# Performance work log

Hardware: AMD Instinct MI355X
Metric: run time of the kernel (lower is better)

Reference implementation:

```python
import jax, jax.numpy as jnp
import numpy as np

B, S, E, H, K, V = 128, 1024, 512, 512, 2, 32000


def setup_inputs() -> dict:
    key = jax.random.key(0)
    k0, k1, k2, k3, k4, k5 = jax.random.split(key, 6)
    scale = 1.0 / np.sqrt(H)  # torch LSTMCell init range
    inp = jax.random.randint(k0, (B, S), 0, V, dtype=jnp.int32)
    input_embed = jax.random.normal(k1, (B, S, E), dtype=jnp.float32)
    # one LSTMCell parameter set per expert cell, stacked on leading K axis
    W_ih = jax.random.uniform(k2, (K, 4 * H, E), jnp.float32, -scale, scale)
    W_hh = jax.random.uniform(k3, (K, 4 * H, H), jnp.float32, -scale, scale)
    b_ih = jax.random.uniform(k4, (K, 4 * H), jnp.float32, -scale, scale)
    b_hh = jax.random.uniform(k5, (K, 4 * H), jnp.float32, -scale, scale)
    return {"input": inp, "input_embed": input_embed,
            "W_ih": W_ih, "W_hh": W_hh, "b_ih": b_ih, "b_hh": b_hh}


def reference(input, input_embed, W_ih, W_hh, b_ih, b_hh):
    # assignments: vocab id -> cell id via modulo (covers the whole vocab)
    num_cells = W_ih.shape[0]
    batch, seq_len, _ = input_embed.shape
    hidden_size = W_hh.shape[-1]
    cell_map = (input % num_cells).astype(jnp.int32)  # [B, S]
    bias = (b_ih + b_hh)[:, None, :]                   # [K, 1, 4H]
    bidx = jnp.arange(batch)

    xs = (jnp.swapaxes(input_embed, 0, 1),  # [S, B, E]
          jnp.swapaxes(cell_map, 0, 1))     # [S, B]

    def step(carry, x):
        h, c = carry
        x_t, k_t = x
        # compute gates for every cell, then pick the routed one per token
        gates = (jnp.einsum('be,kge->kbg', x_t, W_ih)
                 + jnp.einsum('bh,kgh->kbg', h, W_hh)
                 + bias)                      # [K, B, 4H]
        g = gates[k_t, bidx]                  # [B, 4H] routed selection
        i, f, gg, o = jnp.split(g, 4, axis=-1)
        c_new = jax.nn.sigmoid(f) * c + jax.nn.sigmoid(i) * jnp.tanh(gg)
        h_new = jax.nn.sigmoid(o) * jnp.tanh(c_new)
        return (h_new, c_new), h_new

    h0 = jnp.zeros((batch, hidden_size), jnp.float32)
    c0 = jnp.zeros((batch, hidden_size), jnp.float32)
    (h_last, c_last), outs = jax.lax.scan(step, (h0, c0), xs)
    combined_outputs = jnp.swapaxes(outs, 0, 1)  # [B, S, H]
    return combined_outputs, (h_last, c_last)
```

## Files before the change

### kernel.cpp

```cpp
#include <hip/hip_runtime.h>
#include <hip/hip_bf16.h>

typedef __bf16 bf16x8 __attribute__((ext_vector_type(8)));
typedef float f32x4 __attribute__((ext_vector_type(4)));
typedef unsigned long long u64;

#define B_ 128
#define S_ 1024
#define E_ 512
#define H_ 512
#define TOK 32
#define KROWS 64
#define WSTRIDE 1032
#define GSTR 65
#define NGRP 4
#define WPG 64
#define FSTR 16
#define SMEM_BYTES (KROWS * WSTRIDE * 2 + 64 * 4 + TOK * GSTR * 4)

__device__ __forceinline__ float sigf(float x) { return 1.0f / (1.0f + __expf(-x)); }

__device__ __forceinline__ bf16x8 cvt8(float4 a, float4 b) {
    bf16x8 r;
    r[0] = (__bf16)a.x; r[1] = (__bf16)a.y; r[2] = (__bf16)a.z; r[3] = (__bf16)a.w;
    r[4] = (__bf16)b.x; r[5] = (__bf16)b.y; r[6] = (__bf16)b.z; r[7] = (__bf16)b.w;
    return r;
}

union bfpack { u64 q[2]; bf16x8 v; };
union bfbits { __hip_bfloat16 b; unsigned short s; };

__global__ void init_ws_kernel(unsigned int* bar) {
    for (int i = threadIdx.x; i < NGRP * WPG * FSTR; i += 256) bar[i] = 0u;
}

__global__ void __launch_bounds__(512, 2)
lstm_kernel(const int* __restrict__ inp, const float* __restrict__ embed,
            const float* __restrict__ Wih, const float* __restrict__ Whh,
            const float* __restrict__ bih, const float* __restrict__ bhh,
            float* __restrict__ out, unsigned int* __restrict__ bar,
            __hip_bfloat16* __restrict__ hbuf)
{
    extern __shared__ char smem[];
    __hip_bfloat16* wbuf = (__hip_bfloat16*)smem;
    float* bias_l = (float*)(smem + KROWS * WSTRIDE * 2);
    float* gbuf   = bias_l + 64;

    const int tid = threadIdx.x;
    const int bid = blockIdx.x;
    const int grp = bid & 3;
    const int r   = bid >> 2;
    const int j0  = r * 8;

    for (int it = tid; it < KROWS * 256; it += 512) {
        int n = it >> 8;
        int q = it & 255;
        int cell = n >> 5, rem = n & 31, gate = rem >> 3, jj = rem & 7;
        size_t grow = (size_t)(cell * 2048 + gate * 512 + j0 + jj);
        float4 v;
        int dstoff;
        if (q < 128) { v = ((const float4*)(Wih + grow * E_))[q];       dstoff = q * 4; }
        else         { v = ((const float4*)(Whh + grow * H_))[q - 128]; dstoff = 512 + (q - 128) * 4; }
        __hip_bfloat16* dst = wbuf + n * WSTRIDE + dstoff;
        dst[0] = __float2bfloat16(v.x); dst[1] = __float2bfloat16(v.y);
        dst[2] = __float2bfloat16(v.z); dst[3] = __float2bfloat16(v.w);
    }
    if (tid < 64) {
        int n = tid, cell = n >> 5, rem = n & 31, gate = rem >> 3, jj = rem & 7;
        size_t off = (size_t)cell * 2048 + gate * 512 + j0 + jj;
        bias_l[tid] = bih[off] + bhh[off];
    }
    __syncthreads();

    const int lane = tid & 63, wid = tid >> 6;
    const int lm = lane & 15, quad = lane >> 4;
    const int mtile = wid & 1, rho = wid >> 1;
    const int tokA = grp * TOK + mtile * 16 + lm;
    const float* xbase = embed + (size_t)tokA * S_ * E_ + quad * 8;
    const __hip_bfloat16* wx = wbuf + (rho * 16 + lm) * WSTRIDE + quad * 8;
    const __hip_bfloat16* wh = wx + 512;
    const float bv = bias_l[rho * 16 + lm];
    const __hip_bfloat16* hbA = hbuf + (size_t)tokA * H_ + quad * 8;

    const int b_loc = (tid >> 3) & 31, jj = tid & 7;
    const int b_glob = grp * TOK + b_loc;
    const int* inpp = inp + (size_t)b_glob * S_;
    float* outp = out + (size_t)b_glob * S_ * H_ + j0 + jj;
    __hip_bfloat16* hwp = hbuf + (size_t)b_glob * H_ + j0 + jj;
    float creg = 0.0f, hlast = 0.0f;

    volatile unsigned int* myflag = bar + (grp * WPG + r) * FSTR;
    volatile const unsigned int* pollp = bar + (grp * WPG + lane) * FSTR;

    f32x4 acc_next;
    {
        f32x4 ax = {bv, bv, bv, bv};
        const float* xp = xbase;
#pragma unroll
        for (int ks = 0; ks < 16; ++ks) {
            float4 f0 = *(const float4*)(xp + ks * 32);
            float4 f1 = *(const float4*)(xp + ks * 32 + 4);
            bf16x8 a = cvt8(f0, f1);
            bf16x8 b = *(const bf16x8*)(wx + ks * 32);
            ax = __builtin_amdgcn_mfma_f32_16x16x32_bf16(a, b, ax, 0, 0, 0);
        }
        acc_next = ax;
    }
    int cell_next = inpp[0];

    for (int t = 0; t < S_; ++t) {
        f32x4 acc = acc_next;
        const int cell_cur = cell_next;

        if (t > 0) {
            const volatile u64* hp = (const volatile u64*)(hbA + (size_t)(t & 1) * B_ * H_);
#pragma unroll
            for (int ks = 0; ks < 16; ++ks) {
                bfpack u;
                u.q[0] = hp[ks * 8];
                u.q[1] = hp[ks * 8 + 1];
                bf16x8 b = *(const bf16x8*)(wh + ks * 32);
                acc = __builtin_amdgcn_mfma_f32_16x16x32_bf16(u.v, b, acc, 0, 0, 0);
            }
        }

        {
            float* gp = gbuf + (mtile * 16 + quad * 4) * GSTR + rho * 16 + lm;
            gp[0] = acc[0]; gp[GSTR] = acc[1]; gp[2 * GSTR] = acc[2]; gp[3 * GSTR] = acc[3];
        }
        __syncthreads();

        if (tid < 256) {
            int cell = cell_cur & 1;
            const float* gb = gbuf + b_loc * GSTR + cell * 32 + jj;
            float iv = gb[0], fv = gb[8], gv = gb[16], ov = gb[24];
            creg  = sigf(fv) * creg + sigf(iv) * tanhf(gv);
            hlast = sigf(ov) * tanhf(creg);
            bfbits cv; cv.b = __float2bfloat16(hlast);
            *(volatile unsigned short*)(hwp + (size_t)((t + 1) & 1) * B_ * H_) = cv.s;
        }

        __syncthreads();
        if (tid == 0) *myflag = (unsigned int)(t + 1);

        if (tid < 256) outp[(size_t)t * H_] = hlast;
        {
            int tn = (t + 1 < S_) ? (t + 1) : (S_ - 1);
            cell_next = inpp[tn];
        }
        {
            f32x4 ax = {bv, bv, bv, bv};
            if (t + 1 < S_) {
                const float* xp = xbase + (size_t)(t + 1) * E_;
#pragma unroll
                for (int ks = 0; ks < 16; ++ks) {
                    float4 f0 = *(const float4*)(xp + ks * 32);
                    float4 f1 = *(const float4*)(xp + ks * 32 + 4);
                    bf16x8 a = cvt8(f0, f1);
                    bf16x8 b = *(const bf16x8*)(wx + ks * 32);
                    ax = __builtin_amdgcn_mfma_f32_16x16x32_bf16(a, b, ax, 0, 0, 0);
                }
            }
            acc_next = ax;
        }

        if (wid == 0) {
            const unsigned int tgt = (unsigned int)(t + 1);
            unsigned int guard = 0;
            while (!__all((int)(*pollp >= tgt))) {
                __builtin_amdgcn_s_sleep(4);
                if (++guard > 0x02000000u) break;
            }
        }
        __syncthreads();
    }

    if (tid < 256) {
        size_t base = (size_t)B_ * S_ * H_;
        out[base + (size_t)b_glob * H_ + j0 + jj] = hlast;
        out[base + (size_t)B_ * H_ + (size_t)b_glob * H_ + j0 + jj] = creg;
    }
}

extern "C" void kernel_launch(void* const* d_in, const int* in_sizes, int n_in,
                              void* d_out, int out_size, void* d_ws, size_t ws_size,
                              hipStream_t stream) {
    const int* inp     = (const int*)d_in[0];
    const float* embed = (const float*)d_in[1];
    const float* Wih   = (const float*)d_in[2];
    const float* Whh   = (const float*)d_in[3];
    const float* bih   = (const float*)d_in[4];
    const float* bhh   = (const float*)d_in[5];
    float* out         = (float*)d_out;

    unsigned int* bar    = (unsigned int*)d_ws;
    __hip_bfloat16* hbuf = (__hip_bfloat16*)((char*)d_ws + 16384);

    static_assert(SMEM_BYTES <= 160 * 1024, "LDS overflow");
    hipFuncSetAttribute((const void*)lstm_kernel,
                        hipFuncAttributeMaxDynamicSharedMemorySize, SMEM_BYTES);

    hipLaunchKernelGGL(init_ws_kernel, dim3(1), dim3(256), 0, stream, bar);
    hipLaunchKernelGGL(lstm_kernel, dim3(256), dim3(512), SMEM_BYTES, stream,
                       inp, embed, Wih, Whh, bih, bhh, out, bar, hbuf);
}
```

Baseline: 16.77 ms.

## Split hidden columns across 512 workgroups and use hierarchical per-group barrier

Halves the hidden-unit slice per workgroup (4 columns instead of 8), launching 512 workgroups of 256 threads so the grid covers more CUs with smaller LDS weight tiles. The grid-wide step barrier becomes two-level: one leader block per batch group polls all 128 peer flags and then publishes a single group flag that the other blocks poll, with a shorter sleep. This is meant to spread the recurrent matmul and gate work across more compute and to cut polling traffic. In exchange there are more blocks to synchronise and an extra hop of latency through the leader on every timestep.

After: 17.56 ms. 4.7% more time.

```diff
diff --git a/kernel.cpp b/kernel.cpp
--- a/kernel.cpp
+++ b/kernel.cpp
@@ -10,13 +10,14 @@
 #define E_ 512
 #define H_ 512
 #define TOK 32
-#define KROWS 64
+#define KROWS 32
+#define JW 4
 #define WSTRIDE 1032
-#define GSTR 65
+#define GSTR 33
 #define NGRP 4
-#define WPG 64
+#define WPG 128
 #define FSTR 16
-#define SMEM_BYTES (KROWS * WSTRIDE * 2 + 64 * 4 + TOK * GSTR * 4)
+#define SMEM_BYTES (KROWS * WSTRIDE * 2 + KROWS * 4 + TOK * GSTR * 4)
 
 __device__ __forceinline__ float sigf(float x) { return 1.0f / (1.0f + __expf(-x)); }
 
@@ -31,10 +32,10 @@
 union bfbits { __hip_bfloat16 b; unsigned short s; };
 
 __global__ void init_ws_kernel(unsigned int* bar) {
-    for (int i = threadIdx.x; i < NGRP * WPG * FSTR; i += 256) bar[i] = 0u;
-}
-
-__global__ void __launch_bounds__(512, 2)
+    for (int i = threadIdx.x; i < (NGRP * WPG + NGRP) * FSTR; i += 256) bar[i] = 0u;
+}
+
+__global__ void __launch_bounds__(256, 2)
 lstm_kernel(const int* __restrict__ inp, const float* __restrict__ embed,
             const float* __restrict__ Wih, const float* __restrict__ Whh,
             const float* __restrict__ bih, const float* __restrict__ bhh,
@@ -44,19 +45,19 @@
     extern __shared__ char smem[];
     __hip_bfloat16* wbuf = (__hip_bfloat16*)smem;
     float* bias_l = (float*)(smem + KROWS * WSTRIDE * 2);
-    float* gbuf   = bias_l + 64;
+    float* gbuf   = bias_l + KROWS;
 
     const int tid = threadIdx.x;
     const int bid = blockIdx.x;
-    const int grp = bid & 3;
-    const int r   = bid >> 2;
-    const int j0  = r * 8;
-
-    for (int it = tid; it < KROWS * 256; it += 512) {
+    const int grp = (bid + (bid >> 8)) & 3;
+    const int r   = ((bid >> 8) << 6) + ((bid & 255) >> 2);
+    const int j0  = r * JW;
+
+    for (int it = tid; it < KROWS * 256; it += 256) {
         int n = it >> 8;
         int q = it & 255;
-        int cell = n >> 5, rem = n & 31, gate = rem >> 3, jj = rem & 7;
-        size_t grow = (size_t)(cell * 2048 + gate * 512 + j0 + jj);
+        int cell = n >> 4, gate = (n >> 2) & 3, jjj = n & 3;
+        size_t grow = (size_t)(cell * 2048 + gate * 512 + j0 + jjj);
         float4 v;
         int dstoff;
         if (q < 128) { v = ((const float4*)(Wih + grow * E_))[q];       dstoff = q * 4; }
@@ -65,24 +66,24 @@
         dst[0] = __float2bfloat16(v.x); dst[1] = __float2bfloat16(v.y);
         dst[2] = __float2bfloat16(v.z); dst[3] = __float2bfloat16(v.w);
     }
-    if (tid < 64) {
-        int n = tid, cell = n >> 5, rem = n & 31, gate = rem >> 3, jj = rem & 7;
-        size_t off = (size_t)cell * 2048 + gate * 512 + j0 + jj;
+    if (tid < KROWS) {
+        int n = tid, cell = n >> 4, gate = (n >> 2) & 3, jjj = n & 3;
+        size_t off = (size_t)cell * 2048 + gate * 512 + j0 + jjj;
         bias_l[tid] = bih[off] + bhh[off];
     }
     __syncthreads();
 
     const int lane = tid & 63, wid = tid >> 6;
     const int lm = lane & 15, quad = lane >> 4;
-    const int mtile = wid & 1, rho = wid >> 1;
+    const int mtile = wid & 1, ntile = wid >> 1;
     const int tokA = grp * TOK + mtile * 16 + lm;
     const float* xbase = embed + (size_t)tokA * S_ * E_ + quad * 8;
-    const __hip_bfloat16* wx = wbuf + (rho * 16 + lm) * WSTRIDE + quad * 8;
+    const __hip_bfloat16* wx = wbuf + (ntile * 16 + lm) * WSTRIDE + quad * 8;
     const __hip_bfloat16* wh = wx + 512;
-    const float bv = bias_l[rho * 16 + lm];
+    const float bv = bias_l[ntile * 16 + lm];
     const __hip_bfloat16* hbA = hbuf + (size_t)tokA * H_ + quad * 8;
 
-    const int b_loc = (tid >> 3) & 31, jj = tid & 7;
+    const int b_loc = tid >> 2, jj = tid & 3;
     const int b_glob = grp * TOK + b_loc;
     const int* inpp = inp + (size_t)b_glob * S_;
     float* outp = out + (size_t)b_glob * S_ * H_ + j0 + jj;
@@ -90,7 +91,9 @@
     float creg = 0.0f, hlast = 0.0f;
 
     volatile unsigned int* myflag = bar + (grp * WPG + r) * FSTR;
-    volatile const unsigned int* pollp = bar + (grp * WPG + lane) * FSTR;
+    volatile const unsigned int* pf0 = bar + (grp * WPG + lane) * FSTR;
+    volatile const unsigned int* pf1 = pf0 + 64 * FSTR;
+    volatile unsigned int* gop = bar + (NGRP * WPG + grp) * FSTR;
 
     f32x4 acc_next;
     {
@@ -125,15 +128,15 @@
         }
 
         {
-            float* gp = gbuf + (mtile * 16 + quad * 4) * GSTR + rho * 16 + lm;
+            float* gp = gbuf + (mtile * 16 + quad * 4) * GSTR + ntile * 16 + lm;
             gp[0] = acc[0]; gp[GSTR] = acc[1]; gp[2 * GSTR] = acc[2]; gp[3 * GSTR] = acc[3];
         }
         __syncthreads();
 
-        if (tid < 256) {
+        if (tid < 128) {
             int cell = cell_cur & 1;
-            const float* gb = gbuf + b_loc * GSTR + cell * 32 + jj;
-            float iv = gb[0], fv = gb[8], gv = gb[16], ov = gb[24];
+            const float* gb = gbuf + b_loc * GSTR + cell * 16 + jj;
+            float iv = gb[0], fv = gb[4], gv = gb[8], ov = gb[12];
             creg  = sigf(fv) * creg + sigf(iv) * tanhf(gv);
             hlast = sigf(ov) * tanhf(creg);
             bfbits cv; cv.b = __float2bfloat16(hlast);
@@ -143,7 +146,7 @@
         __syncthreads();
         if (tid == 0) *myflag = (unsigned int)(t + 1);
 
-        if (tid < 256) outp[(size_t)t * H_] = hlast;
+        if (tid < 128) outp[(size_t)t * H_] = hlast;
         {
             int tn = (t + 1 < S_) ? (t + 1) : (S_ - 1);
             cell_next = inpp[tn];
@@ -167,15 +170,23 @@
         if (wid == 0) {
             const unsigned int tgt = (unsigned int)(t + 1);
             unsigned int guard = 0;
-            while (!__all((int)(*pollp >= tgt))) {
-                __builtin_amdgcn_s_sleep(4);
-                if (++guard > 0x02000000u) break;
+            if (r == 0) {
+                while (!__all((int)(*pf0 >= tgt) & (int)(*pf1 >= tgt))) {
+                    __builtin_amdgcn_s_sleep(2);
+                    if (++guard > 0x02000000u) break;
+                }
+                if (lane == 0) *gop = tgt;
+            } else {
+                while (*gop < tgt) {
+                    __builtin_amdgcn_s_sleep(2);
+                    if (++guard > 0x02000000u) break;
+                }
             }
         }
         __syncthreads();
     }
 
-    if (tid < 256) {
+    if (tid < 128) {
         size_t base = (size_t)B_ * S_ * H_;
         out[base + (size_t)b_glob * H_ + j0 + jj] = hlast;
         out[base + (size_t)B_ * H_ + (size_t)b_glob * H_ + j0 + jj] = creg;
@@ -194,13 +205,13 @@
     float* out         = (float*)d_out;
 
     unsigned int* bar    = (unsigned int*)d_ws;
-    __hip_bfloat16* hbuf = (__hip_bfloat16*)((char*)d_ws + 16384);
-
-    static_assert(SMEM_BYTES <= 160 * 1024, "LDS overflow");
+    __hip_bfloat16* hbuf = (__hip_bfloat16*)((char*)d_ws + 36864);
+
+    static_assert(SMEM_BYTES <= 80 * 1024, "LDS too big for 2 wgs/CU");
     hipFuncSetAttribute((const void*)lstm_kernel,
                         hipFuncAttributeMaxDynamicSharedMemorySize, SMEM_BYTES);
 
     hipLaunchKernelGGL(init_ws_kernel, dim3(1), dim3(256), 0, stream, bar);
-    hipLaunchKernelGGL(lstm_kernel, dim3(256), dim3(512), SMEM_BYTES, stream,
+    hipLaunchKernelGGL(lstm_kernel, dim3(512), dim3(256), SMEM_BYTES, stream,
                        inp, embed, Wih, Whh, bih, bhh, out, bar, hbuf);
 }
```
